# Kernel tuning notes

Measured on AMD Instinct MI355X. Metric: run time of the kernel, lower is better.

The kernel has to match this reference:

```python
import jax, jax.numpy as jnp
import numpy as np

# Dims: B latent vectors processed through T sequential LALR-state calls.
B, T = 4096, 128      # batch of latent vecs, timesteps
NL = 256              # n_latent (scaled up from default 100)
NS = 64               # number of LALR states with learned layers
NO = 32               # output tokens per state (Linear(n_latent, n_out))
V = 64                # len(terminals): size of scattered output vector


def setup_inputs() -> dict:
    key = jax.random.key(0)
    ks = jax.random.split(key, 7)
    return {
        "latent0": jax.random.normal(ks[0], (B, NL), jnp.float32),
        "W1": jax.random.normal(ks[1], (NS, NL, NL), jnp.float32) / np.sqrt(NL).astype(np.float32),
        "b1": jax.random.normal(ks[2], (NS, NL), jnp.float32) * 0.01,
        "W2": jax.random.normal(ks[3], (NS, NO, NL), jnp.float32) / np.sqrt(NL).astype(np.float32),
        "b2": jax.random.normal(ks[4], (NS, NO), jnp.float32) * 0.01,
        "state_seq": jax.random.randint(ks[5], (T,), 0, NS, jnp.int32),
        "out_idx": jax.random.randint(ks[6], (NS, NO), 0, V, jnp.int32),
    }


def reference(latent0, W1, b1, W2, b2, state_seq, out_idx):
    """Per-timestep LALR state call:
       newlatent = tanh(Linear(x));
       probs     = softmax(Linear(newlatent));
       output    = IndicesExpansion: scatter probs into zeros(V) at out_idx[state].
    State weights are gathered by state id; batch is processed jointly."""
    def step(x, s):
        w1, bb1 = W1[s], b1[s]            # [NL,NL], [NL]
        w2, bb2 = W2[s], b2[s]            # [NO,NL], [NO]
        idx = out_idx[s]                  # [NO]
        x_new = jnp.tanh(x @ w1.T + bb1)                       # [B, NL]
        probs = jax.nn.softmax(x_new @ w2.T + bb2, axis=-1)    # [B, NO]
        # IndicesExpansionLayer: zero vector of size V, set vals at indices
        y = jnp.zeros((x.shape[0], V), x.dtype).at[:, idx].set(probs)
        return x_new, y

    final_latent, ys = jax.lax.scan(step, latent0, state_seq)  # ys: [T, B, V]
    return jnp.transpose(ys, (1, 0, 2))  # [B, T, V]
```

## Files before the change

kernel.cpp:

```cpp
#include <hip/hip_runtime.h>

#define B_  4096
#define T_  128
#define NL  256
#define NS  64
#define NO  32
#define V_  64
#define RB  16
#define NBLK (B_ / RB)

typedef __bf16 bf16;
typedef bf16  bf16x8 __attribute__((ext_vector_type(8)));
typedef bf16  bf16x4 __attribute__((ext_vector_type(4)));
typedef float f32x4  __attribute__((ext_vector_type(4)));

#define MF(a, b, c) __builtin_amdgcn_mfma_f32_16x16x32_bf16(a, b, c, 0, 0, 0)

template <int TSHIFT>
__global__ void split_w_frag(const float* __restrict__ src,
                             bf16* __restrict__ hi, bf16* __restrict__ lo,
                             int total4) {
    int t4 = blockIdx.x * blockDim.x + threadIdx.x;
    if (t4 >= total4) return;
    const int jb   = (t4 & 1) * 4;
    const int L    = (t4 >> 1) & 63;
    const int ks   = (t4 >> 7) & 7;
    const int rest = t4 >> 10;
    const int t    = rest & ((1 << TSHIFT) - 1);
    const int s    = rest >> TSHIFT;
    const int row  = ((s << TSHIFT) + t) * 16 + (L & 15);
    const int k    = ks * 32 + (L >> 4) * 8 + jb;
    const float4 v = *(const float4*)(src + (size_t)row * NL + k);
    float vv[4] = {v.x, v.y, v.z, v.w};
    bf16x4 h, l;
#pragma unroll
    for (int e = 0; e < 4; e++) {
        bf16 hh = (bf16)vv[e];
        h[e] = hh;
        l[e] = (bf16)(vv[e] - (float)hh);
    }
    *(bf16x4*)(hi + (size_t)t4 * 4) = h;
    *(bf16x4*)(lo + (size_t)t4 * 4) = l;
}

__global__ void inv_kernel(const int* __restrict__ out_idx, int* __restrict__ inv) {
    int t = blockIdx.x * blockDim.x + threadIdx.x;
    if (t >= NS * V_) return;
    int s = t >> 6, v = t & 63;
    int jf = -1;
#pragma unroll
    for (int j = 0; j < NO; j++)
        if (out_idx[(s << 5) | j] == v) jf = j;
    inv[t] = jf;
}

__device__ __forceinline__ float fast_tanh(float z) {
    float e = __expf(2.0f * z);
    return 1.0f - 2.0f / (e + 1.0f);
}

__device__ __forceinline__ int xaddr(int t, int q, int n) {
    return ((t >> 1) * 512) + (((t & 1) * 2 + (q >> 1)) * 128) + n * 8 + (q & 1) * 4;
}

__launch_bounds__(1024, 4)
__global__ void lalr_main(const float* __restrict__ latent0,
                          const float* __restrict__ b1,
                          const float* __restrict__ b2,
                          const int*   __restrict__ state_seq,
                          const int*   __restrict__ inv,
                          const bf16*  __restrict__ W1h, const bf16* __restrict__ W1l,
                          const bf16*  __restrict__ W2h, const bf16* __restrict__ W2l,
                          float* __restrict__ out) {
    __shared__ bf16  xh[2][4096];
    __shared__ bf16  xl[2][4096];
    __shared__ float Sp[2][8][16][36];

    const int tid  = threadIdx.x;
    const int wave = tid >> 6;
    const int lane = tid & 63;
    const int n    = lane & 15;
    const int q    = lane >> 4;
    const int r0   = blockIdx.x * RB;
    const int t2   = wave & 1;
    const int ks2  = wave >> 1;

    {
        float4 v = *(const float4*)(latent0 + (size_t)(r0 + n) * NL + wave * 16 + q * 4);
        float vv[4] = {v.x, v.y, v.z, v.w};
        bf16x4 hv, lv;
#pragma unroll
        for (int e = 0; e < 4; e++) {
            bf16 hh = (bf16)vv[e];
            hv[e] = hh;
            lv[e] = (bf16)(vv[e] - (float)hh);
        }
        const int a = xaddr(wave, q, n);
        *(bf16x4*)(&xh[0][a]) = hv;
        *(bf16x4*)(&xl[0][a]) = lv;
    }

    int s0 = state_seq[0], s1 = -1, s2 = -1;

    bf16x8 pwh[4], pwl[4];
    const bf16* w1hb = W1h + ((size_t)(s0 * 16 + wave) * 8) * 512;
    const bf16* w1lb = W1l + ((size_t)(s0 * 16 + wave) * 8) * 512;
#pragma unroll
    for (int p = 0; p < 4; p++) {
        pwh[p] = *(const bf16x8*)(w1hb + p * 512 + lane * 8);
        pwl[p] = *(const bf16x8*)(w1lb + p * 512 + lane * 8);
    }
    bf16x8 w2h2, w2l2;

    __syncthreads();

    for (int i = 0; i <= T_ + 1; i++) {
        const int ib = i & 1;
        const int cur = ib;

        f32x4 acc1;
        if (s0 >= 0) {
            acc1 = (f32x4){0.f, 0.f, 0.f, 0.f};
#pragma unroll
            for (int ks = 0; ks < 8; ks++) {
                bf16x8 xa = *(const bf16x8*)(&xh[cur][ks * 512 + lane * 8]);
                bf16x8 xb = *(const bf16x8*)(&xl[cur][ks * 512 + lane * 8]);
                const int sl = ks & 3;
                bf16x8 wh = pwh[sl], wl = pwl[sl];
                if (ks < 4) {
                    pwh[sl] = *(const bf16x8*)(w1hb + (ks + 4) * 512 + lane * 8);
                    pwl[sl] = *(const bf16x8*)(w1lb + (ks + 4) * 512 + lane * 8);
                }
                acc1 = MF(wh, xa, acc1);
                acc1 = MF(wl, xa, acc1);
                acc1 = MF(wh, xb, acc1);
            }
        }

        if (s1 >= 0) {
            bf16x8 xa = *(const bf16x8*)(&xh[cur][ks2 * 512 + lane * 8]);
            bf16x8 xb = *(const bf16x8*)(&xl[cur][ks2 * 512 + lane * 8]);
            f32x4 a2 = (f32x4){0.f, 0.f, 0.f, 0.f};
            a2 = MF(w2h2, xa, a2);
            a2 = MF(w2l2, xa, a2);
            a2 = MF(w2h2, xb, a2);
            if (ks2 == 0) {
                float4 bb = *(const float4*)(b2 + s1 * NO + t2 * 16 + q * 4);
                a2[0] += bb.x; a2[1] += bb.y; a2[2] += bb.z; a2[3] += bb.w;
            }
            *(f32x4*)(&Sp[ib][ks2][n][t2 * 16 + q * 4]) = a2;
        }

        const int ns0 = (i + 1 < T_) ? state_seq[i + 1] : -1;
        if (s0 >= 0) {
            const bf16* w2hb = W2h + ((size_t)((s0 * 2 + t2) * 8 + ks2)) * 512;
            const bf16* w2lb = W2l + ((size_t)((s0 * 2 + t2) * 8 + ks2)) * 512;
            w2h2 = *(const bf16x8*)(w2hb + lane * 8);
            w2l2 = *(const bf16x8*)(w2lb + lane * 8);
        }
        if (ns0 >= 0) {
            w1hb = W1h + ((size_t)(ns0 * 16 + wave) * 8) * 512;
            w1lb = W1l + ((size_t)(ns0 * 16 + wave) * 8) * 512;
#pragma unroll
            for (int p = 0; p < 4; p++) {
                pwh[p] = *(const bf16x8*)(w1hb + p * 512 + lane * 8);
                pwl[p] = *(const bf16x8*)(w1lb + p * 512 + lane * 8);
            }
        }

        if (s2 >= 0 && tid < 256) {
            const int r  = tid >> 4;
            const int j0 = tid & 15;
            const int pb = (i - 1) & 1;
            float v0 = 0.f, v1 = 0.f;
#pragma unroll
            for (int w = 0; w < 8; w++) {
                v0 += Sp[pb][w][r][j0];
                v1 += Sp[pb][w][r][j0 + 16];
            }
            float m = fmaxf(v0, v1);
#pragma unroll
            for (int d = 1; d < 16; d <<= 1) m = fmaxf(m, __shfl_xor(m, d));
            float e0 = __expf(v0 - m), e1 = __expf(v1 - m);
            float su = e0 + e1;
#pragma unroll
            for (int d = 1; d < 16; d <<= 1) su += __shfl_xor(su, d);
            float is = 1.0f / su;
            float p0 = e0 * is, p1 = e1 * is;
            const int gb = lane & 48;
            int4 iv4 = *(const int4*)(inv + s2 * V_ + j0 * 4);
            int ivv[4] = {iv4.x, iv4.y, iv4.z, iv4.w};
            float o[4];
#pragma unroll
            for (int e = 0; e < 4; e++) {
                float ga = __shfl(p0, gb + (ivv[e] & 15));
                float gc = __shfl(p1, gb + (ivv[e] & 15));
                o[e] = (ivv[e] < 0) ? 0.f : ((ivv[e] < 16) ? ga : gc);
            }
            *(float4*)(out + ((size_t)(r0 + r) * T_ + (i - 2)) * V_ + j0 * 4) = *(float4*)o;
        }

        if (s0 >= 0) {
            float4 bb = *(const float4*)(b1 + s0 * NL + wave * 16 + q * 4);
            float bv[4] = {bb.x, bb.y, bb.z, bb.w};
            bf16x4 hv, lv;
#pragma unroll
            for (int e = 0; e < 4; e++) {
                float h = fast_tanh(acc1[e] + bv[e]);
                bf16 hh = (bf16)h;
                hv[e] = hh;
                lv[e] = (bf16)(h - (float)hh);
            }
            const int a = xaddr(wave, q, n);
            *(bf16x4*)(&xh[cur ^ 1][a]) = hv;
            *(bf16x4*)(&xl[cur ^ 1][a]) = lv;
        }

        s2 = s1; s1 = s0; s0 = ns0;
        __syncthreads();
    }
}

extern "C" void kernel_launch(void* const* d_in, const int* in_sizes, int n_in,
                              void* d_out, int out_size, void* d_ws, size_t ws_size,
                              hipStream_t stream) {
    const float* latent0   = (const float*)d_in[0];
    const float* W1        = (const float*)d_in[1];
    const float* b1        = (const float*)d_in[2];
    const float* W2        = (const float*)d_in[3];
    const float* b2        = (const float*)d_in[4];
    const int*   state_seq = (const int*)d_in[5];
    const int*   out_idx   = (const int*)d_in[6];
    float* out = (float*)d_out;

    bf16* W1h = (bf16*)d_ws;
    bf16* W1l = W1h + (size_t)NS * NL * NL;
    bf16* W2h = W1l + (size_t)NS * NL * NL;
    bf16* W2l = W2h + (size_t)NS * NO * NL;
    int*  inv = (int*)(W2l + (size_t)NS * NO * NL);

    const int n4_w1 = NS * NL * NL / 4;
    const int n4_w2 = NS * NO * NL / 4;
    split_w_frag<4><<<n4_w1 / 256, 256, 0, stream>>>(W1, W1h, W1l, n4_w1);
    split_w_frag<1><<<n4_w2 / 256, 256, 0, stream>>>(W2, W2h, W2l, n4_w2);
    inv_kernel<<<(NS * V_ + 255) / 256, 256, 0, stream>>>(out_idx, inv);

    lalr_main<<<NBLK, 1024, 0, stream>>>(latent0, b1, b2, state_seq, inv,
                                         W1h, W1l, W2h, W2l, out);
}
```

Measured before the change: 580.2 us.

## Prefetch full next-state W1 fragments in registers and use lighter LDS barrier

Each wave now holds all eight W1 hi/lo fragments in registers and, as it consumes each fragment in the MFMA loop, loads the matching fragment for the next timestep's state. Before, only half were double-buffered and the rest were reloaded after the loop. The b1 bias load is also hoisted to the start of the iteration. The __syncthreads barrier is replaced by an inline s_waitcnt lgkmcnt(0) plus s_barrier, which does not wait for outstanding global loads, so the prefetches can stay in flight across the barrier. This doubles the register footprint for W1 fragments, which may lower occupancy, and the inline-asm barrier relies on the compiler inserting waits before the prefetched registers are used.

```diff
diff --git a/kernel.cpp b/kernel.cpp
--- a/kernel.cpp
+++ b/kernel.cpp
@@ -15,6 +15,10 @@
 typedef float f32x4  __attribute__((ext_vector_type(4)));
 
 #define MF(a, b, c) __builtin_amdgcn_mfma_f32_16x16x32_bf16(a, b, c, 0, 0, 0)
+
+__device__ __forceinline__ void block_sync_lds() {
+    asm volatile("s_waitcnt lgkmcnt(0)\ns_barrier" ::: "memory");
+}
 
 template <int TSHIFT>
 __global__ void split_w_frag(const float* __restrict__ src,
@@ -102,21 +106,31 @@
 
     int s0 = state_seq[0], s1 = -1, s2 = -1;
 
-    bf16x8 pwh[4], pwl[4];
-    const bf16* w1hb = W1h + ((size_t)(s0 * 16 + wave) * 8) * 512;
-    const bf16* w1lb = W1l + ((size_t)(s0 * 16 + wave) * 8) * 512;
-#pragma unroll
-    for (int p = 0; p < 4; p++) {
-        pwh[p] = *(const bf16x8*)(w1hb + p * 512 + lane * 8);
-        pwl[p] = *(const bf16x8*)(w1lb + p * 512 + lane * 8);
+    bf16x8 pwh[8], pwl[8];
+    {
+        const bf16* w1hb = W1h + ((size_t)(s0 * 16 + wave) * 8) * 512;
+        const bf16* w1lb = W1l + ((size_t)(s0 * 16 + wave) * 8) * 512;
+#pragma unroll
+        for (int p = 0; p < 8; p++) {
+            pwh[p] = *(const bf16x8*)(w1hb + p * 512 + lane * 8);
+            pwl[p] = *(const bf16x8*)(w1lb + p * 512 + lane * 8);
+        }
     }
     bf16x8 w2h2, w2l2;
 
-    __syncthreads();
+    block_sync_lds();
 
     for (int i = 0; i <= T_ + 1; i++) {
-        const int ib = i & 1;
+        const int ib  = i & 1;
         const int cur = ib;
+
+        const int ns0 = (i + 1 < T_) ? state_seq[i + 1] : -1;
+        const int pfs = (ns0 >= 0) ? ns0 : 0;
+        const bf16* nw1hb = W1h + ((size_t)(pfs * 16 + wave) * 8) * 512;
+        const bf16* nw1lb = W1l + ((size_t)(pfs * 16 + wave) * 8) * 512;
+
+        float4 bb1;
+        if (s0 >= 0) bb1 = *(const float4*)(b1 + s0 * NL + wave * 16 + q * 4);
 
         f32x4 acc1;
         if (s0 >= 0) {
@@ -125,12 +139,9 @@
             for (int ks = 0; ks < 8; ks++) {
                 bf16x8 xa = *(const bf16x8*)(&xh[cur][ks * 512 + lane * 8]);
                 bf16x8 xb = *(const bf16x8*)(&xl[cur][ks * 512 + lane * 8]);
-                const int sl = ks & 3;
-                bf16x8 wh = pwh[sl], wl = pwl[sl];
-                if (ks < 4) {
-                    pwh[sl] = *(const bf16x8*)(w1hb + (ks + 4) * 512 + lane * 8);
-                    pwl[sl] = *(const bf16x8*)(w1lb + (ks + 4) * 512 + lane * 8);
-                }
+                bf16x8 wh = pwh[ks], wl = pwl[ks];
+                pwh[ks] = *(const bf16x8*)(nw1hb + ks * 512 + lane * 8);
+                pwl[ks] = *(const bf16x8*)(nw1lb + ks * 512 + lane * 8);
                 acc1 = MF(wh, xa, acc1);
                 acc1 = MF(wl, xa, acc1);
                 acc1 = MF(wh, xb, acc1);
@@ -151,21 +162,11 @@
             *(f32x4*)(&Sp[ib][ks2][n][t2 * 16 + q * 4]) = a2;
         }
 
-        const int ns0 = (i + 1 < T_) ? state_seq[i + 1] : -1;
         if (s0 >= 0) {
             const bf16* w2hb = W2h + ((size_t)((s0 * 2 + t2) * 8 + ks2)) * 512;
             const bf16* w2lb = W2l + ((size_t)((s0 * 2 + t2) * 8 + ks2)) * 512;
             w2h2 = *(const bf16x8*)(w2hb + lane * 8);
             w2l2 = *(const bf16x8*)(w2lb + lane * 8);
-        }
-        if (ns0 >= 0) {
-            w1hb = W1h + ((size_t)(ns0 * 16 + wave) * 8) * 512;
-            w1lb = W1l + ((size_t)(ns0 * 16 + wave) * 8) * 512;
-#pragma unroll
-            for (int p = 0; p < 4; p++) {
-                pwh[p] = *(const bf16x8*)(w1hb + p * 512 + lane * 8);
-                pwl[p] = *(const bf16x8*)(w1lb + p * 512 + lane * 8);
-            }
         }
 
         if (s2 >= 0 && tid < 256) {
@@ -201,8 +202,7 @@
         }
 
         if (s0 >= 0) {
-            float4 bb = *(const float4*)(b1 + s0 * NL + wave * 16 + q * 4);
-            float bv[4] = {bb.x, bb.y, bb.z, bb.w};
+            float bv[4] = {bb1.x, bb1.y, bb1.z, bb1.w};
             bf16x4 hv, lv;
 #pragma unroll
             for (int e = 0; e < 4; e++) {
@@ -217,7 +217,7 @@
         }
 
         s2 = s1; s1 = s0; s0 = ns0;
-        __syncthreads();
+        block_sync_lds();
     }
 }
 
```

Result: slower. 702.8 us (+21.1%).
